# Optimization experiments

Measured on AMD Instinct MI355X. Metric: run time of the kernel, lower is better.

The kernel has to match this reference:

```python
import jax, jax.numpy as jnp
import numpy as np

HEAD_SIZE = 64
EMBED_DIM = 1024
N_HEAD = EMBED_DIM // HEAD_SIZE
BATCH, SEQ = 8, 2048


def wkv6(r, k, v, w, u, s):
    # r,k,v,w: (B,T,H,D); u: (H,D); s: (B,H,D,D) indexed state[j,i] (j: key dim, i: value dim)
    decay = jnp.exp(-jnp.exp(w))  # RWKV-6 CUDA kernel computes exp(-exp(w)) per channel/step

    def step(state, inp):
        r_t, k_t, v_t, d_t = inp  # each (B,H,D)
        kv = k_t[..., :, None] * v_t[..., None, :]  # (B,H,D,D)
        y_t = jnp.einsum('bhj,bhji->bhi', r_t, state + u[..., :, None] * kv)
        state = d_t[..., :, None] * state + kv
        return state, y_t

    xs = tuple(jnp.moveaxis(t, 1, 0) for t in (r, k, v, decay))  # time-major (T,B,H,D)
    s_final, y = jax.lax.scan(step, s, xs)
    return jnp.moveaxis(y, 0, 1), s_final  # (B,T,H,D), (B,H,D,D)


def setup_inputs() -> dict:
    key = jax.random.key(0)
    ks = jax.random.split(key, 20)
    C, H, D = EMBED_DIM, N_HEAD, HEAD_SIZE
    f = jnp.float32
    inp = {
        'x': jax.random.normal(ks[0], (BATCH, SEQ, C), f),
        'x_last': jax.random.normal(ks[1], (BATCH, SEQ, C), f),
        's': jnp.zeros((BATCH, H, D, D), f),
        'miu_x': jax.random.uniform(ks[2], (1, 1, C), f),
        'lambda_': jax.random.uniform(ks[3], (5, 1, 1, C), f),
        'A': jax.random.normal(ks[4], (C, 160), f) * 0.01,
        'B_lora': jax.random.normal(ks[5], (5, 32, C), f) * 0.01,
        'time_decay_miu': jax.random.uniform(ks[6], (1, 1, C), f, minval=-6.0, maxval=-0.5),
        'td_A': jax.random.normal(ks[7], (C, 64), f) * 0.01,
        'td_B': jax.random.normal(ks[8], (64, C), f) * 0.01,
        'u': jax.random.normal(ks[9], (H, D), f) * 0.5,
        'W_k': jax.random.normal(ks[10], (C, C), f) * (0.05 / C ** 0.5),
        'W_v': jax.random.normal(ks[11], (C, C), f) * (0.5 / C ** 0.5),
        'W_r': jax.random.normal(ks[12], (C, C), f) * (0.5 / C ** 0.5),
        'W_o': jax.random.normal(ks[13], (C, C), f) * (0.5 / C ** 0.5),
        'W_g1': jax.random.normal(ks[14], (C, 160), f) * 0.01,
        'W_g2': jax.random.normal(ks[15], (160, C), f) * 0.01,
        'gn_gamma': jnp.ones((C,), f),
        'gn_beta': jnp.zeros((C,), f),
    }
    return inp


def reference(x, x_last, s, miu_x, lambda_, A, B_lora, time_decay_miu, td_A, td_B, u,
              W_k, W_v, W_r, W_o, W_g1, W_g2, gn_gamma, gn_beta):
    Bsz, T, C = x.shape
    H, D = C // HEAD_SIZE, HEAD_SIZE
    x_raw = x
    # ddlerp: token-shift mix with data-dependent mus from batched LoRA
    b_a = x_last - x
    xl = x + b_a * miu_x
    # NB: source uses a raw .view(5, B*T, 32) (no transpose) -- replicate exactly with reshape
    t1 = jnp.tanh(xl @ A).reshape(5, Bsz * T, 32)
    miu = lambda_ + jnp.einsum('fmk,fkc->fmc', t1, B_lora).reshape(5, Bsz, T, C)
    xdd = x[None] + b_a[None] * miu  # (5,B,T,C)
    w0, k0, v0, r0, g0 = xdd[0], xdd[1], xdd[2], xdd[3], xdd[4]
    # decay LoRA
    w = time_decay_miu + jnp.tanh(w0 @ td_A) @ td_B  # (B,T,C)
    k = (k0 @ W_k.T) * jnp.exp(jnp.minimum(w, 0.0))
    v = v0 @ W_v.T
    r = r0 @ W_r.T
    g = jnp.tanh(g0 @ W_g1) @ W_g2
    rh, kh, vh, wh = (t.reshape(Bsz, T, H, D) for t in (r, k, v, w))
    y, s_new = wkv6(rh, kh, vh, wh, u, s)
    # GroupNorm over (B*T, n_head groups of head_size), eps = 1e-5 * n_head
    y = y.reshape(Bsz * T, H, D)
    eps = 1e-5 * H
    mu = y.mean(axis=-1, keepdims=True)
    var = y.var(axis=-1, keepdims=True)
    yn = (y - mu) / jnp.sqrt(var + eps)
    yn = yn * gn_gamma.reshape(H, D) + gn_beta.reshape(H, D)
    yn = yn.reshape(Bsz, T, C)
    out = (yn * g) @ W_o.T
    return out, x_raw, s_new
```

## Files before the change

### kernel.cpp

```cpp
#include <hip/hip_runtime.h>
#include <hip/hip_bf16.h>

namespace {

typedef __attribute__((ext_vector_type(8))) short short8x;
typedef __attribute__((ext_vector_type(4))) float f32x4;

__device__ __forceinline__ float bf2f(unsigned short h) {
    return __uint_as_float(((unsigned int)h) << 16);
}
__device__ __forceinline__ unsigned short f2bf(float f) {
    __hip_bfloat16 h = __float2bfloat16(f);
    return *reinterpret_cast<unsigned short*>(&h);
}

enum { ACT_NONE = 0, ACT_TANH = 1 };
enum { EPI_NONE = 0, EPI_KSCALE = 1, EPI_ADDVEC = 2 };

template <int ACT, int EPI, int SBF>
__launch_bounds__(256) __global__
void gemm_mfma(int Npad, int K, int Nreal, int Cstride,
               const unsigned short* __restrict__ A,
               const unsigned short* __restrict__ B,
               float* __restrict__ Cf, unsigned short* __restrict__ Cb,
               const float* __restrict__ epi)
{
    __shared__ unsigned short as_[128 * 32];
    __shared__ unsigned short bs_[128 * 32];
    const int tid = threadIdx.x;
    const int lane = tid & 63;
    const int wave = tid >> 6;
    const int m0 = blockIdx.y << 7;
    const int n0 = blockIdx.x << 7;
    const int wm = (wave >> 1) << 6;
    const int wn = (wave & 1) << 6;

    f32x4 acc[4][4];
    const f32x4 zero = {0.f, 0.f, 0.f, 0.f};
#pragma unroll
    for (int i = 0; i < 4; ++i)
#pragma unroll
        for (int j = 0; j < 4; ++j) acc[i][j] = zero;

    const int sr = tid >> 2;
    const int sc4 = tid & 3;

    for (int k0 = 0; k0 < K; k0 += 32) {
        const uint4 a0 = *(const uint4*)(A + (size_t)(m0 + sr) * K + k0 + sc4 * 8);
        const uint4 a1 = *(const uint4*)(A + (size_t)(m0 + 64 + sr) * K + k0 + sc4 * 8);
        const uint4 b0 = *(const uint4*)(B + (size_t)(n0 + sr) * K + k0 + sc4 * 8);
        const uint4 b1 = *(const uint4*)(B + (size_t)(n0 + 64 + sr) * K + k0 + sc4 * 8);
        __syncthreads();
        {
            int r = sr, p = sc4 ^ ((r >> 1) & 3);
            *(uint4*)&as_[r * 32 + p * 8] = a0;
            *(uint4*)&bs_[r * 32 + p * 8] = b0;
            r = 64 + sr; p = sc4 ^ ((r >> 1) & 3);
            *(uint4*)&as_[r * 32 + p * 8] = a1;
            *(uint4*)&bs_[r * 32 + p * 8] = b1;
        }
        __syncthreads();
        const int q = lane >> 4;
        const int l15 = lane & 15;
        short8x af[4], bfr[4];
#pragma unroll
        for (int i = 0; i < 4; ++i) {
            const int m = wm + (i << 4) + l15;
            const int pa = q ^ ((m >> 1) & 3);
            af[i] = *(const short8x*)&as_[m * 32 + pa * 8];
            const int n = wn + (i << 4) + l15;
            const int pb = q ^ ((n >> 1) & 3);
            bfr[i] = *(const short8x*)&bs_[n * 32 + pb * 8];
        }
#pragma unroll
        for (int i = 0; i < 4; ++i)
#pragma unroll
            for (int j = 0; j < 4; ++j)
                acc[i][j] = __builtin_amdgcn_mfma_f32_16x16x32_bf16(af[i], bfr[j], acc[i][j], 0, 0, 0);
    }

    const int q = lane >> 4;
    const int cn = lane & 15;
#pragma unroll
    for (int i = 0; i < 4; ++i) {
#pragma unroll
        for (int j = 0; j < 4; ++j) {
#pragma unroll
            for (int rr = 0; rr < 4; ++rr) {
                const int row = m0 + wm + (i << 4) + (q << 2) + rr;
                const int col = n0 + wn + (j << 4) + cn;
                if (col >= Nreal) continue;
                float v = acc[i][j][rr];
                if constexpr (ACT == ACT_TANH) v = tanhf(v);
                if constexpr (EPI == EPI_KSCALE)
                    v *= __expf(fminf(epi[(size_t)row * 1024 + col], 0.f));
                if constexpr (EPI == EPI_ADDVEC) v += epi[col];
                if constexpr (SBF) Cb[(size_t)row * Cstride + col] = f2bf(v);
                else               Cf[(size_t)row * Cstride + col] = v;
            }
        }
    }
}

__launch_bounds__(256) __global__
void mix_k(const float* __restrict__ x, const float* __restrict__ xla,
           const float* __restrict__ mux, unsigned short* __restrict__ out)
{
    const size_t idx = ((size_t)blockIdx.x * 256 + threadIdx.x) * 4;
    const int c = (int)(idx & 1023);
    const float4 xv = *(const float4*)(x + idx);
    const float4 xl = *(const float4*)(xla + idx);
    const float4 mu = *(const float4*)(mux + c);
    ushort4 o;
    o.x = f2bf(xv.x + (xl.x - xv.x) * mu.x);
    o.y = f2bf(xv.y + (xl.y - xv.y) * mu.y);
    o.z = f2bf(xv.z + (xl.z - xv.z) * mu.z);
    o.w = f2bf(xv.w + (xl.w - xv.w) * mu.w);
    *(ushort4*)(out + idx) = o;
}

__launch_bounds__(256) __global__
void convert_k(const float* __restrict__ src, unsigned short* __restrict__ dst)
{
    const size_t idx = ((size_t)blockIdx.x * 256 + threadIdx.x) * 4;
    const float4 v = *(const float4*)(src + idx);
    ushort4 o;
    o.x = f2bf(v.x); o.y = f2bf(v.y); o.z = f2bf(v.z); o.w = f2bf(v.w);
    *(ushort4*)(dst + idx) = o;
}

__launch_bounds__(256) __global__
void transpose_k(const float* __restrict__ src, unsigned short* __restrict__ dst,
                 int K, int Nsrc)
{
    const int k = blockIdx.x * 256 + threadIdx.x;
    const int n = blockIdx.y;
    if (k < K)
        dst[(size_t)n * K + k] = (n < Nsrc) ? f2bf(src[(size_t)k * Nsrc + n]) : (unsigned short)0;
}

__launch_bounds__(256) __global__
void xdd_k(const float* __restrict__ x, const float* __restrict__ xla,
           const unsigned short* __restrict__ t1, const float* __restrict__ blora,
           const float* __restrict__ lam, unsigned short* __restrict__ out, int f)
{
    __shared__ float sh[4][32];
    const int tid = threadIdx.x;
    const int m0 = blockIdx.x << 2;
    if (tid < 128) {
        const int r = tid >> 5, kk = tid & 31;
        sh[r][kk] = bf2f(t1[(size_t)f * 524288 + (size_t)(m0 + r) * 32 + kk]);
    }
    __syncthreads();
    const int c0 = tid << 2;
    const float* bl = blora + f * 32768 + c0;
    float dot[4][4];
#pragma unroll
    for (int r = 0; r < 4; ++r)
#pragma unroll
        for (int j = 0; j < 4; ++j) dot[r][j] = 0.f;
    for (int kk = 0; kk < 32; ++kk) {
        const float4 b4 = *(const float4*)(bl + (size_t)kk * 1024);
#pragma unroll
        for (int r = 0; r < 4; ++r) {
            const float tv = sh[r][kk];
            dot[r][0] = fmaf(tv, b4.x, dot[r][0]);
            dot[r][1] = fmaf(tv, b4.y, dot[r][1]);
            dot[r][2] = fmaf(tv, b4.z, dot[r][2]);
            dot[r][3] = fmaf(tv, b4.w, dot[r][3]);
        }
    }
    const float4 l4 = *(const float4*)(lam + f * 1024 + c0);
#pragma unroll
    for (int r = 0; r < 4; ++r) {
        const size_t idx = (size_t)(m0 + r) * 1024 + c0;
        const float4 xv = *(const float4*)(x + idx);
        const float4 xl = *(const float4*)(xla + idx);
        ushort4 o;
        o.x = f2bf(xv.x + (xl.x - xv.x) * (l4.x + dot[r][0]));
        o.y = f2bf(xv.y + (xl.y - xv.y) * (l4.y + dot[r][1]));
        o.z = f2bf(xv.z + (xl.z - xv.z) * (l4.z + dot[r][2]));
        o.w = f2bf(xv.w + (xl.w - xv.w) * (l4.w + dot[r][3]));
        *(ushort4*)(out + idx) = o;
    }
}

__launch_bounds__(256) __global__
void decay_k(float* __restrict__ p)
{
    const size_t idx = ((size_t)blockIdx.x * 256 + threadIdx.x) * 4;
    const float4 v = *(const float4*)(p + idx);
    float4 o;
    o.x = __expf(-__expf(v.x));
    o.y = __expf(-__expf(v.y));
    o.z = __expf(-__expf(v.z));
    o.w = __expf(-__expf(v.w));
    *(float4*)(p + idx) = o;
}

#define BF_LO(x) __uint_as_float((x) << 16)
#define BF_HI(x) __uint_as_float((x) & 0xFFFF0000u)

#define WKV_LOAD(RV, KV, DV, VVv, T0)                                         \
    do {                                                                      \
        _Pragma("unroll")                                                     \
        for (int tt = 0; tt < 4; ++tt) {                                      \
            const size_t o_ = (size_t)((T0) + tt) * 1024;                     \
            RV[tt] = *(const uint4*)(rp + o_);                                \
            KV[tt] = *(const uint4*)(kp + o_);                                \
            DV[tt][0] = *(const float4*)(dp + o_);                            \
            DV[tt][1] = *(const float4*)(dp + o_ + 4);                        \
            VVv[tt] = vp[o_];                                                 \
        }                                                                     \
    } while (0)

#define P3_PROC(RV, KV, DV, VVv, SLOT, T0)                                    \
    do {                                                                      \
        _Pragma("unroll")                                                     \
        for (int tt = 0; tt < 4; ++tt) {                                      \
            const float vi_ = bf2f(VVv[tt]);                                  \
            float rj[8], kj[8], dj[8];                                        \
            rj[0] = BF_LO(RV[tt].x); rj[1] = BF_HI(RV[tt].x);                 \
            rj[2] = BF_LO(RV[tt].y); rj[3] = BF_HI(RV[tt].y);                 \
            rj[4] = BF_LO(RV[tt].z); rj[5] = BF_HI(RV[tt].z);                 \
            rj[6] = BF_LO(RV[tt].w); rj[7] = BF_HI(RV[tt].w);                 \
            kj[0] = BF_LO(KV[tt].x); kj[1] = BF_HI(KV[tt].x);                 \
            kj[2] = BF_LO(KV[tt].y); kj[3] = BF_HI(KV[tt].y);                 \
            kj[4] = BF_LO(KV[tt].z); kj[5] = BF_HI(KV[tt].z);                 \
            kj[6] = BF_LO(KV[tt].w); kj[7] = BF_HI(KV[tt].w);                 \
            dj[0] = DV[tt][0].x; dj[1] = DV[tt][0].y;                         \
            dj[2] = DV[tt][0].z; dj[3] = DV[tt][0].w;                         \
            dj[4] = DV[tt][1].x; dj[5] = DV[tt][1].y;                         \
            dj[6] = DV[tt][1].z; dj[7] = DV[tt][1].w;                         \
            float ya0_ = 0.f, ya1_ = 0.f;                                     \
            _Pragma("unroll")                                                 \
            for (int jj = 0; jj < 8; ++jj) {                                  \
                const float t_ = kj[jj] * vi_;                                \
                const float a_ = fmaf(u8[jj], t_, s[jj]);                     \
                if (jj & 1) ya1_ = fmaf(rj[jj], a_, ya1_);                    \
                else        ya0_ = fmaf(rj[jj], a_, ya0_);                    \
                s[jj] = fmaf(dj[jj], s[jj], t_);                              \
            }                                                                 \
            red[SLOT][w][tt][l] = ya0_ + ya1_;                                \
        }                                                                     \
        __syncthreads();                                                      \
        if (w < 4) {                                                          \
            float acc_ = red[SLOT][0][w][l];                                  \
            _Pragma("unroll")                                                 \
            for (int w_ = 1; w_ < 8; ++w_) acc_ += red[SLOT][w_][w][l];       \
            yp[(size_t)((T0) + w) * 1024] = acc_;                             \
        }                                                                     \
    } while (0)

#define P1_LOAD(KV, DV, VVv, T0)                                              \
    do {                                                                      \
        _Pragma("unroll")                                                     \
        for (int tt = 0; tt < 4; ++tt) {                                      \
            const size_t o_ = (size_t)((T0) + tt) * 1024;                     \
            KV[tt] = *(const uint4*)(kp + o_);                                \
            DV[tt][0] = *(const float4*)(dp + o_);                            \
            DV[tt][1] = *(const float4*)(dp + o_ + 4);                        \
            VVv[tt] = vp[o_];                                                 \
        }                                                                     \
    } while (0)

#define P1_PROC(KV, DV, VVv)                                                  \
    do {                                                                      \
        _Pragma("unroll")                                                     \
        for (int tt = 0; tt < 4; ++tt) {                                      \
            const float vi_ = bf2f(VVv[tt]);                                  \
            float kj[8], dj[8];                                               \
            kj[0] = BF_LO(KV[tt].x); kj[1] = BF_HI(KV[tt].x);                 \
            kj[2] = BF_LO(KV[tt].y); kj[3] = BF_HI(KV[tt].y);                 \
            kj[4] = BF_LO(KV[tt].z); kj[5] = BF_HI(KV[tt].z);                 \
            kj[6] = BF_LO(KV[tt].w); kj[7] = BF_HI(KV[tt].w);                 \
            dj[0] = DV[tt][0].x; dj[1] = DV[tt][0].y;                         \
            dj[2] = DV[tt][0].z; dj[3] = DV[tt][0].w;                         \
            dj[4] = DV[tt][1].x; dj[5] = DV[tt][1].y;                         \
            dj[6] = DV[tt][1].z; dj[7] = DV[tt][1].w;                         \
            _Pragma("unroll")                                                 \
            for (int jj = 0; jj < 8; ++jj) {                                  \
                const float t_ = kj[jj] * vi_;                                \
                s[jj] = fmaf(dj[jj], s[jj], t_);                              \
                D[jj] *= dj[jj];                                              \
            }                                                                 \
        }                                                                     \
    } while (0)

__launch_bounds__(64) __global__
void wkv_p1(const unsigned short* __restrict__ k, const unsigned short* __restrict__ v,
            const float* __restrict__ d,
            float* __restrict__ slocal, float* __restrict__ dprod)
{
    const int blk = blockIdx.x;
    const int bh = blk & 127;
    const int jc = (blk >> 7) & 7;
    const int tc = blk >> 10;
    const int h = bh & 15;
    const int l = threadIdx.x;
    const int jbase = jc << 3;

    float s[8], D[8];
#pragma unroll
    for (int jj = 0; jj < 8; ++jj) { s[jj] = 0.f; D[jj] = 1.f; }

    const size_t base = (size_t)(bh >> 4) * (2048 * 1024) + (size_t)tc * 131072 + (h << 6);
    const unsigned short* kp = k + base + jbase;
    const float*          dp = d + base + jbase;
    const unsigned short* vp = v + base + l;

    uint4 kA[4]; float4 dA[4][2]; unsigned short vA[4];
    uint4 kB[4]; float4 dB[4][2]; unsigned short vB[4];

    P1_LOAD(kA, dA, vA, 0);
    for (int c = 0; c < 32; c += 2) {
        P1_LOAD(kB, dB, vB, (c + 1) * 4);
        P1_PROC(kA, dA, vA);
        if (c + 2 < 32) P1_LOAD(kA, dA, vA, (c + 2) * 4);
        P1_PROC(kB, dB, vB);
    }
    const size_t cb = (size_t)(tc * 128 + bh) * 64 + jbase;
#pragma unroll
    for (int jj = 0; jj < 8; ++jj) slocal[(cb + jj) * 64 + l] = s[jj];
    if (l == 0) {
#pragma unroll
        for (int jj = 0; jj < 8; ++jj) dprod[cb + jj] = D[jj];
    }
}

__launch_bounds__(64) __global__
void wkv_p2(const float* __restrict__ s_in, const float* __restrict__ slocal,
            const float* __restrict__ dprod, float* __restrict__ sstart,
            float* __restrict__ s_out)
{
    const int blk = blockIdx.x;
    const int bh = blk & 127;
    const int jc = blk >> 7;
    const int l = threadIdx.x;
    const int jbase = jc << 3;

    float s[8];
    const size_t sb = (size_t)bh * 4096;
#pragma unroll
    for (int jj = 0; jj < 8; ++jj) s[jj] = s_in[sb + (size_t)(jbase + jj) * 64 + l];

    for (int c = 0; c < 16; ++c) {
        const size_t cb = (size_t)(c * 128 + bh) * 64 + jbase;
#pragma unroll
        for (int jj = 0; jj < 8; ++jj) sstart[(cb + jj) * 64 + l] = s[jj];
#pragma unroll
        for (int jj = 0; jj < 8; ++jj)
            s[jj] = fmaf(dprod[cb + jj], s[jj], slocal[(cb + jj) * 64 + l]);
    }
#pragma unroll
    for (int jj = 0; jj < 8; ++jj) s_out[sb + (size_t)(jbase + jj) * 64 + l] = s[jj];
}

__launch_bounds__(512) __global__
void wkv_p3(const unsigned short* __restrict__ r, const unsigned short* __restrict__ k,
            const unsigned short* __restrict__ v, const float* __restrict__ d,
            const float* __restrict__ u, const float* __restrict__ sstart,
            float* __restrict__ y)
{
    const int blk = blockIdx.x;
    const int bh = blk & 127;
    const int tc = blk >> 7;
    const int h = bh & 15;
    const int tid = threadIdx.x;
    const int w = tid >> 6;
    const int l = tid & 63;
    const int jbase = w << 3;

    __shared__ float red[2][8][4][64];

    float s[8];
    const size_t cb = (size_t)(tc * 128 + bh) * 64 + jbase;
#pragma unroll
    for (int jj = 0; jj < 8; ++jj) s[jj] = sstart[(cb + jj) * 64 + l];

    float u8[8];
#pragma unroll
    for (int jj = 0; jj < 8; ++jj) u8[jj] = u[(h << 6) + jbase + jj];

    const size_t base = (size_t)(bh >> 4) * (2048 * 1024) + (size_t)tc * 131072 + (h << 6);
    const unsigned short* rp = r + base + jbase;
    const unsigned short* kp = k + base + jbase;
    const float*          dp = d + base + jbase;
    const unsigned short* vp = v + base + l;
    float*                yp = y + base + l;

    uint4 rA[4], kA[4]; float4 dA[4][2]; unsigned short vA[4];
    uint4 rB[4], kB[4]; float4 dB[4][2]; unsigned short vB[4];

    WKV_LOAD(rA, kA, dA, vA, 0);
    for (int c = 0; c < 32; c += 2) {
        WKV_LOAD(rB, kB, dB, vB, (c + 1) * 4);
        P3_PROC(rA, kA, dA, vA, 0, c * 4);
        if (c + 2 < 32) WKV_LOAD(rA, kA, dA, vA, (c + 2) * 4);
        P3_PROC(rB, kB, dB, vB, 1, (c + 1) * 4);
    }
}

__launch_bounds__(256) __global__
void gn_k(const float* __restrict__ y0,
          const unsigned short* __restrict__ g, const float* __restrict__ gam,
          const float* __restrict__ bet, unsigned short* __restrict__ z)
{
    const int tid = threadIdx.x;
    const size_t row = blockIdx.x;
    const int c0 = tid << 2;
    const size_t idx = row * 1024 + c0;
    const float4 a = *(const float4*)(y0 + idx);
    const float yv0 = a.x, yv1 = a.y, yv2 = a.z, yv3 = a.w;
    float sm = yv0 + yv1 + yv2 + yv3;
    float q = yv0 * yv0 + yv1 * yv1 + yv2 * yv2 + yv3 * yv3;
#pragma unroll
    for (int off = 1; off < 16; off <<= 1) {
        sm += __shfl_xor(sm, off, 64);
        q += __shfl_xor(q, off, 64);
    }
    const float mean = sm * (1.f / 64.f);
    const float var = q * (1.f / 64.f) - mean * mean;
    const float rstd = rsqrtf(var + 1.6e-4f);
    const float4 gm = *(const float4*)(gam + c0);
    const float4 bt = *(const float4*)(bet + c0);
    const ushort4 gg = *(const ushort4*)(g + idx);
    ushort4 o;
    o.x = f2bf(((yv0 - mean) * rstd * gm.x + bt.x) * bf2f(gg.x));
    o.y = f2bf(((yv1 - mean) * rstd * gm.y + bt.y) * bf2f(gg.y));
    o.z = f2bf(((yv2 - mean) * rstd * gm.z + bt.z) * bf2f(gg.z));
    o.w = f2bf(((yv3 - mean) * rstd * gm.w + bt.w) * bf2f(gg.w));
    *(ushort4*)(z + idx) = o;
}

__launch_bounds__(256) __global__
void copy_k(const float4* __restrict__ src, float4* __restrict__ dst)
{
    const size_t i = (size_t)blockIdx.x * 256 + threadIdx.x;
    dst[i] = src[i];
}

}

extern "C" void kernel_launch(void* const* d_in, const int* in_sizes, int n_in,
                              void* d_out, int out_size, void* d_ws, size_t ws_size,
                              hipStream_t stream)
{
    (void)in_sizes; (void)n_in; (void)out_size; (void)ws_size;
    const float* x     = (const float*)d_in[0];
    const float* xla   = (const float*)d_in[1];
    const float* s_in  = (const float*)d_in[2];
    const float* mux   = (const float*)d_in[3];
    const float* lam   = (const float*)d_in[4];
    const float* Amat  = (const float*)d_in[5];
    const float* blora = (const float*)d_in[6];
    const float* tdmu  = (const float*)d_in[7];
    const float* tdA   = (const float*)d_in[8];
    const float* tdB   = (const float*)d_in[9];
    const float* u     = (const float*)d_in[10];
    const float* Wk    = (const float*)d_in[11];
    const float* Wv    = (const float*)d_in[12];
    const float* Wr    = (const float*)d_in[13];
    const float* Wo    = (const float*)d_in[14];
    const float* Wg1   = (const float*)d_in[15];
    const float* Wg2   = (const float*)d_in[16];
    const float* gam   = (const float*)d_in[17];
    const float* bet   = (const float*)d_in[18];

    float* out  = (float*)d_out;
    float* xraw = out + 16777216;
    float* snew = out + 2 * 16777216;

    char* ws = (char*)d_ws;
    unsigned short* mixb   = (unsigned short*)(ws);
    unsigned short* xddb   = (unsigned short*)(ws + 33554432);
    unsigned short* t1     = (unsigned short*)(ws + 67108864);
    unsigned short* tanh64 = (unsigned short*)(ws + 72351744);
    unsigned short* tanhg  = (unsigned short*)(ws + 74448896);
    unsigned short* kbuf   = (unsigned short*)(ws + 79691776);
    unsigned short* vbuf   = (unsigned short*)(ws + 113246208);
    unsigned short* rbuf   = (unsigned short*)(ws + 146800640);
    unsigned short* gbuf   = (unsigned short*)(ws + 180355072);
    unsigned short* wkt    = (unsigned short*)(ws + 213909504);
    unsigned short* wvt    = (unsigned short*)(ws + 216006656);
    unsigned short* wrt    = (unsigned short*)(ws + 218103808);
    unsigned short* wot    = (unsigned short*)(ws + 220200960);
    unsigned short* at_    = (unsigned short*)(ws + 222298112);
    unsigned short* tdat   = (unsigned short*)(ws + 222822400);
    unsigned short* tdbt   = (unsigned short*)(ws + 223084544);
    unsigned short* wg1t   = (unsigned short*)(ws + 223215616);
    unsigned short* wg2t   = (unsigned short*)(ws + 223739904);

    float* w  = out;
    float* y0 = xraw;
    float* slocal = (float*)ws;
    float* sstart = (float*)(ws + 33554432);
    float* dprod  = (float*)(ws + 67108864);

    convert_k<<<1024, 256, 0, stream>>>(Wk, wkt);
    convert_k<<<1024, 256, 0, stream>>>(Wv, wvt);
    convert_k<<<1024, 256, 0, stream>>>(Wr, wrt);
    convert_k<<<1024, 256, 0, stream>>>(Wo, wot);
    transpose_k<<<dim3(4, 256), 256, 0, stream>>>(Amat, at_, 1024, 160);
    transpose_k<<<dim3(4, 128), 256, 0, stream>>>(tdA, tdat, 1024, 64);
    transpose_k<<<dim3(1, 1024), 256, 0, stream>>>(tdB, tdbt, 64, 1024);
    transpose_k<<<dim3(4, 256), 256, 0, stream>>>(Wg1, wg1t, 1024, 160);
    transpose_k<<<dim3(1, 1024), 256, 0, stream>>>(Wg2, wg2t, 160, 1024);

    mix_k<<<16384, 256, 0, stream>>>(x, xla, mux, mixb);
    gemm_mfma<ACT_TANH, EPI_NONE, 1><<<dim3(2, 128), 256, 0, stream>>>(
        256, 1024, 160, 160, mixb, at_, nullptr, t1, nullptr);

    xdd_k<<<4096, 256, 0, stream>>>(x, xla, t1, blora, lam, xddb, 0);
    gemm_mfma<ACT_TANH, EPI_NONE, 1><<<dim3(1, 128), 256, 0, stream>>>(
        128, 1024, 64, 64, xddb, tdat, nullptr, tanh64, nullptr);
    gemm_mfma<ACT_NONE, EPI_ADDVEC, 0><<<dim3(8, 128), 256, 0, stream>>>(
        1024, 64, 1024, 1024, tanh64, tdbt, w, nullptr, tdmu);

    xdd_k<<<4096, 256, 0, stream>>>(x, xla, t1, blora, lam, xddb, 1);
    gemm_mfma<ACT_NONE, EPI_KSCALE, 1><<<dim3(8, 128), 256, 0, stream>>>(
        1024, 1024, 1024, 1024, xddb, wkt, nullptr, kbuf, w);

    decay_k<<<16384, 256, 0, stream>>>(w);

    xdd_k<<<4096, 256, 0, stream>>>(x, xla, t1, blora, lam, xddb, 2);
    gemm_mfma<ACT_NONE, EPI_NONE, 1><<<dim3(8, 128), 256, 0, stream>>>(
        1024, 1024, 1024, 1024, xddb, wvt, nullptr, vbuf, nullptr);

    xdd_k<<<4096, 256, 0, stream>>>(x, xla, t1, blora, lam, xddb, 3);
    gemm_mfma<ACT_NONE, EPI_NONE, 1><<<dim3(8, 128), 256, 0, stream>>>(
        1024, 1024, 1024, 1024, xddb, wrt, nullptr, rbuf, nullptr);

    xdd_k<<<4096, 256, 0, stream>>>(x, xla, t1, blora, lam, xddb, 4);
    gemm_mfma<ACT_TANH, EPI_NONE, 1><<<dim3(2, 128), 256, 0, stream>>>(
        256, 1024, 160, 160, xddb, wg1t, nullptr, tanhg, nullptr);
    gemm_mfma<ACT_NONE, EPI_NONE, 1><<<dim3(8, 128), 256, 0, stream>>>(
        1024, 160, 1024, 1024, tanhg, wg2t, nullptr, gbuf, nullptr);

    wkv_p1<<<16384, 64, 0, stream>>>(kbuf, vbuf, w, slocal, dprod);
    wkv_p2<<<1024, 64, 0, stream>>>(s_in, slocal, dprod, sstart, snew);
    wkv_p3<<<2048, 512, 0, stream>>>(rbuf, kbuf, vbuf, w, u, sstart, y0);

    gn_k<<<16384, 256, 0, stream>>>(y0, gbuf, gam, bet, kbuf);

    gemm_mfma<ACT_NONE, EPI_NONE, 0><<<dim3(8, 128), 256, 0, stream>>>(
        1024, 1024, 1024, 1024, kbuf, wot, out, nullptr, nullptr);

    copy_k<<<16384, 256, 0, stream>>>((const float4*)x, (float4*)xraw);
}
```

Measured before the change: 1.602 ms.

## Use direct global-to-LDS loads in GEMM, batch WKV reductions, split decay product

```diff
diff --git a/kernel.cpp b/kernel.cpp
--- a/kernel.cpp
+++ b/kernel.cpp
@@ -12,6 +12,11 @@
 __device__ __forceinline__ unsigned short f2bf(float f) {
     __hip_bfloat16 h = __float2bfloat16(f);
     return *reinterpret_cast<unsigned short*>(&h);
+}
+__device__ __forceinline__ void gload16(const unsigned short* g, unsigned short* l) {
+    __builtin_amdgcn_global_load_lds(
+        (const __attribute__((address_space(1))) void*)g,
+        (__attribute__((address_space(3))) void*)l, 16, 0, 0);
 }
 
 enum { ACT_NONE = 0, ACT_TANH = 1 };
@@ -42,35 +47,31 @@
 #pragma unroll
         for (int j = 0; j < 4; ++j) acc[i][j] = zero;
 
-    const int sr = tid >> 2;
-    const int sc4 = tid & 3;
+    const int grow = lane >> 2;
+    const int gcol = (lane & 3) << 3;
+    const unsigned short* a0p = A + (size_t)(m0 + (wave << 5) + grow) * K + gcol;
+    const unsigned short* a1p = A + (size_t)(m0 + (wave << 5) + 16 + grow) * K + gcol;
+    const unsigned short* b0p = B + (size_t)(n0 + (wave << 5) + grow) * K + gcol;
+    const unsigned short* b1p = B + (size_t)(n0 + (wave << 5) + 16 + grow) * K + gcol;
+    unsigned short* la0 = as_ + (wave * 2 + 0) * 512;
+    unsigned short* la1 = as_ + (wave * 2 + 1) * 512;
+    unsigned short* lb0 = bs_ + (wave * 2 + 0) * 512;
+    unsigned short* lb1 = bs_ + (wave * 2 + 1) * 512;
 
     for (int k0 = 0; k0 < K; k0 += 32) {
-        const uint4 a0 = *(const uint4*)(A + (size_t)(m0 + sr) * K + k0 + sc4 * 8);
-        const uint4 a1 = *(const uint4*)(A + (size_t)(m0 + 64 + sr) * K + k0 + sc4 * 8);
-        const uint4 b0 = *(const uint4*)(B + (size_t)(n0 + sr) * K + k0 + sc4 * 8);
-        const uint4 b1 = *(const uint4*)(B + (size_t)(n0 + 64 + sr) * K + k0 + sc4 * 8);
         __syncthreads();
-        {
-            int r = sr, p = sc4 ^ ((r >> 1) & 3);
-            *(uint4*)&as_[r * 32 + p * 8] = a0;
-            *(uint4*)&bs_[r * 32 + p * 8] = b0;
-            r = 64 + sr; p = sc4 ^ ((r >> 1) & 3);
-            *(uint4*)&as_[r * 32 + p * 8] = a1;
-            *(uint4*)&bs_[r * 32 + p * 8] = b1;
-        }
+        gload16(a0p + k0, la0);
+        gload16(b0p + k0, lb0);
+        gload16(a1p + k0, la1);
+        gload16(b1p + k0, lb1);
         __syncthreads();
         const int q = lane >> 4;
         const int l15 = lane & 15;
         short8x af[4], bfr[4];
 #pragma unroll
         for (int i = 0; i < 4; ++i) {
-            const int m = wm + (i << 4) + l15;
-            const int pa = q ^ ((m >> 1) & 3);
-            af[i] = *(const short8x*)&as_[m * 32 + pa * 8];
-            const int n = wn + (i << 4) + l15;
-            const int pb = q ^ ((n >> 1) & 3);
-            bfr[i] = *(const short8x*)&bs_[n * 32 + pb * 8];
+            af[i]  = *(const short8x*)&as_[(wm + (i << 4) + l15) * 32 + q * 8];
+            bfr[i] = *(const short8x*)&bs_[(wn + (i << 4) + l15) * 32 + q * 8];
         }
 #pragma unroll
         for (int i = 0; i < 4; ++i)
@@ -214,7 +215,7 @@
         }                                                                     \
     } while (0)
 
-#define P3_PROC(RV, KV, DV, VVv, SLOT, T0)                                    \
+#define P3_COMP(RV, KV, DV, VVv, SLOT, TH)                                    \
     do {                                                                      \
         _Pragma("unroll")                                                     \
         for (int tt = 0; tt < 4; ++tt) {                                      \
@@ -241,14 +242,7 @@
                 else        ya0_ = fmaf(rj[jj], a_, ya0_);                    \
                 s[jj] = fmaf(dj[jj], s[jj], t_);                              \
             }                                                                 \
-            red[SLOT][w][tt][l] = ya0_ + ya1_;                                \
-        }                                                                     \
-        __syncthreads();                                                      \
-        if (w < 4) {                                                          \
-            float acc_ = red[SLOT][0][w][l];                                  \
-            _Pragma("unroll")                                                 \
-            for (int w_ = 1; w_ < 8; ++w_) acc_ += red[SLOT][w_][w][l];       \
-            yp[(size_t)((T0) + w) * 1024] = acc_;                             \
+            red[SLOT][w][(TH) * 4 + tt][l] = ya0_ + ya1_;                     \
         }                                                                     \
     } while (0)
 
@@ -259,7 +253,7 @@
             const size_t o_ = (size_t)((T0) + tt) * 1024;                     \
             KV[tt] = *(const uint4*)(kp + o_);                                \
             DV[tt][0] = *(const float4*)(dp + o_);                            \
-            DV[tt][1] = *(const float4*)(dp + o_ + 4);                        \
+            DV[tt][1] = *(const float4*)(dp + o_ + 4);                       \
             VVv[tt] = vp[o_];                                                 \
         }                                                                     \
     } while (0)
@@ -282,15 +276,13 @@
             for (int jj = 0; jj < 8; ++jj) {                                  \
                 const float t_ = kj[jj] * vi_;                                \
                 s[jj] = fmaf(dj[jj], s[jj], t_);                              \
-                D[jj] *= dj[jj];                                              \
             }                                                                 \
         }                                                                     \
     } while (0)
 
 __launch_bounds__(64) __global__
 void wkv_p1(const unsigned short* __restrict__ k, const unsigned short* __restrict__ v,
-            const float* __restrict__ d,
-            float* __restrict__ slocal, float* __restrict__ dprod)
+            const float* __restrict__ d, float* __restrict__ slocal)
 {
     const int blk = blockIdx.x;
     const int bh = blk & 127;
@@ -300,9 +292,9 @@
     const int l = threadIdx.x;
     const int jbase = jc << 3;
 
-    float s[8], D[8];
-#pragma unroll
-    for (int jj = 0; jj < 8; ++jj) { s[jj] = 0.f; D[jj] = 1.f; }
+    float s[8];
+#pragma unroll
+    for (int jj = 0; jj < 8; ++jj) s[jj] = 0.f;
 
     const size_t base = (size_t)(bh >> 4) * (2048 * 1024) + (size_t)tc * 131072 + (h << 6);
     const unsigned short* kp = k + base + jbase;
@@ -322,10 +314,25 @@
     const size_t cb = (size_t)(tc * 128 + bh) * 64 + jbase;
 #pragma unroll
     for (int jj = 0; jj < 8; ++jj) slocal[(cb + jj) * 64 + l] = s[jj];
-    if (l == 0) {
-#pragma unroll
-        for (int jj = 0; jj < 8; ++jj) dprod[cb + jj] = D[jj];
-    }
+}
+
+__launch_bounds__(64) __global__
+void dprod_k(const float* __restrict__ d, float* __restrict__ dprod)
+{
+    const int blk = blockIdx.x;
+    const int bh = blk & 127;
+    const int tc = blk >> 7;
+    const int h = bh & 15;
+    const int l = threadIdx.x;
+    const size_t base = (size_t)(bh >> 4) * (2048 * 1024) + (size_t)tc * 131072 + (h << 6) + l;
+    float d0 = 1.f, d1 = 1.f, d2 = 1.f, d3 = 1.f;
+    for (int t = 0; t < 128; t += 4) {
+        d0 *= d[base + (size_t)t * 1024];
+        d1 *= d[base + (size_t)(t + 1) * 1024];
+        d2 *= d[base + (size_t)(t + 2) * 1024];
+        d3 *= d[base + (size_t)(t + 3) * 1024];
+    }
+    dprod[(size_t)blk * 64 + l] = (d0 * d1) * (d2 * d3);
 }
 
 __launch_bounds__(64) __global__
@@ -371,7 +378,7 @@
     const int l = tid & 63;
     const int jbase = w << 3;
 
-    __shared__ float red[2][8][4][64];
+    __shared__ float red[2][8][8][64];
 
     float s[8];
     const size_t cb = (size_t)(tc * 128 + bh) * 64 + jbase;
@@ -393,11 +400,17 @@
     uint4 rB[4], kB[4]; float4 dB[4][2]; unsigned short vB[4];
 
     WKV_LOAD(rA, kA, dA, vA, 0);
-    for (int c = 0; c < 32; c += 2) {
-        WKV_LOAD(rB, kB, dB, vB, (c + 1) * 4);
-        P3_PROC(rA, kA, dA, vA, 0, c * 4);
-        if (c + 2 < 32) WKV_LOAD(rA, kA, dA, vA, (c + 2) * 4);
-        P3_PROC(rB, kB, dB, vB, 1, (c + 1) * 4);
+    for (int g = 0; g < 16; ++g) {
+        const int t0 = g * 8;
+        WKV_LOAD(rB, kB, dB, vB, t0 + 4);
+        P3_COMP(rA, kA, dA, vA, g & 1, 0);
+        if (g + 1 < 16) WKV_LOAD(rA, kA, dA, vA, t0 + 8);
+        P3_COMP(rB, kB, dB, vB, g & 1, 1);
+        __syncthreads();
+        float acc_ = red[g & 1][0][w][l];
+#pragma unroll
+        for (int w_ = 1; w_ < 8; ++w_) acc_ += red[g & 1][w_][w][l];
+        yp[(size_t)(t0 + w) * 1024] = acc_;
     }
 }
 
@@ -537,7 +550,8 @@
     gemm_mfma<ACT_NONE, EPI_NONE, 1><<<dim3(8, 128), 256, 0, stream>>>(
         1024, 160, 1024, 1024, tanhg, wg2t, nullptr, gbuf, nullptr);
 
-    wkv_p1<<<16384, 64, 0, stream>>>(kbuf, vbuf, w, slocal, dprod);
+    wkv_p1<<<16384, 64, 0, stream>>>(kbuf, vbuf, w, slocal);
+    dprod_k<<<2048, 64, 0, stream>>>(w, dprod);
     wkv_p2<<<1024, 64, 0, stream>>>(s_in, slocal, dprod, sstart, snew);
     wkv_p3<<<2048, 512, 0, stream>>>(rbuf, kbuf, vbuf, w, u, sstart, y0);
 
```

Result: faster. 1.570 ms (-2.0%).
